# Performance work log

Hardware: AMD Instinct MI355X
Metric: run time of the kernel (lower is better)

The kernel has to match this reference:

```python
import jax, jax.numpy as jnp
import numpy as np

PH, PW = 7, 7      # pool_shape
SCALE = 1.0        # spatial_scale of PrRoIPool2D


def _tent_int(t):
    """Antiderivative of the bilinear tent kernel max(0, 1-|t|), clipped.
    Integral of tent from -inf to t."""
    t = jnp.clip(t, -1.0, 1.0)
    return jnp.where(t < 0.0, 0.5 * (t + 1.0) ** 2, 1.0 - 0.5 * (1.0 - t) ** 2)


def _axis_weights(lo, hi, n_bins, size):
    """Exact per-pixel integration weights along one axis.
    lo, hi: [R] roi edges. Returns (w [R, n_bins, size], bin_size [R]).
    w[r,k,i] = integral over bin k of tent(x - i) dx, so that
    sum_i F[i] * w[r,k,i] is the exact integral of the linearly
    interpolated signal F over bin k (Precise RoI Pooling)."""
    binsz = (hi - lo) / n_bins                       # [R]
    k = jnp.arange(n_bins, dtype=lo.dtype)
    a = lo[:, None] + k[None, :] * binsz[:, None]    # [R, n_bins] bin starts
    b = a + binsz[:, None]                           # bin ends
    i = jnp.arange(size, dtype=lo.dtype)             # pixel coordinates
    w = _tent_int(b[:, :, None] - i[None, None, :]) - _tent_int(a[:, :, None] - i[None, None, :])
    return w, binsz


def setup_inputs() -> dict:
    key = jax.random.key(0)
    k1, k2, k3, k4, k5 = jax.random.split(key, 5)
    B, C, H, W = 8, 64, 64, 64
    N = 512  # rois per leading dim; total R = N * B = 4096
    feature = jax.random.normal(k1, (B, C, H, W), dtype=jnp.float32)
    bidx = jax.random.randint(k2, (N, B, 1, 1), 0, B).astype(jnp.float32)
    x1 = jax.random.uniform(k3, (N, B, 1, 1), minval=0.0, maxval=W - 12.0)
    y1 = jax.random.uniform(k4, (N, B, 1, 1), minval=0.0, maxval=H - 12.0)
    wh = jax.random.uniform(k5, (N, B, 1, 1, 2), minval=4.0, maxval=12.0)
    x2 = x1 + wh[..., 0]
    y2 = y1 + wh[..., 1]
    rois = jnp.stack([bidx, x1, y1, x2, y2], axis=-1)  # [N, B, 1, 1, 5]
    return {"feature": feature, "rois": rois}


def reference(feature, rois):
    B, C, H, W = feature.shape
    # rois.permute([1,0,2,3,4]).reshape(-1, 5)
    r = jnp.transpose(rois, (1, 0, 2, 3, 4)).reshape(-1, 5)  # [R, 5]
    bidx = r[:, 0].astype(jnp.int32)
    x1 = r[:, 1] * SCALE
    y1 = r[:, 2] * SCALE
    x2 = r[:, 3] * SCALE
    y2 = r[:, 4] * SCALE

    wx, bw = _axis_weights(x1, x2, PW, W)  # [R, PW, W], [R]
    wy, bh = _axis_weights(y1, y2, PH, H)  # [R, PH, H], [R]

    # Route each ROI to its feature-batch entry without materializing
    # a [R, C, H, W] gather: fold the batch one-hot into the y-weights.
    onehot = (bidx[:, None] == jnp.arange(B)[None, :]).astype(feature.dtype)  # [R, B]
    wy_b = wy[:, :, None, :] * onehot[:, None, :, None]                      # [R, PH, B, H]

    tmp = jnp.einsum('rubi,bcij->rucj', wy_b, feature)  # [R, PH, C, W]
    integ = jnp.einsum('rucj,rvj->rcuv', tmp, wx)       # [R, C, PH, PW]

    area = jnp.maximum(bw * bh, 0.0)[:, None, None, None]
    bins = jnp.where(area > 0, integ / jnp.maximum(area, 1e-12), 0.0)

    # AvgPool2d(pool_shape) over the full (PH, PW) grid -> [R, C, 1, 1]
    out = jnp.mean(bins, axis=(2, 3), keepdims=True)
    return out
```

## Files before the change

kernel.cpp:

```cpp
#include <hip/hip_runtime.h>

constexpr int B = 8, C = 64, H = 64, W = 64;
constexpr int N = 512;
constexpr int R = N * B;
constexpr int HW = H * W;

__device__ __forceinline__ float tent_int(float t) {
    t = fminf(1.0f, fmaxf(-1.0f, t));
    float u = t + 1.0f;
    float v = 1.0f - t;
    return (t < 0.0f) ? 0.5f * u * u : 1.0f - 0.5f * v * v;
}

__global__ __launch_bounds__(256) void transpose_kernel(
    const float* __restrict__ in,
    float* __restrict__ out)
{
    __shared__ float tile[64][65];
    const int b  = blockIdx.x >> 6;
    const int tp = (blockIdx.x & 63) * 64;
    const int t  = threadIdx.x;
    const int tq = t >> 6;
    const int tl = t & 63;

    const float* src = in + (size_t)b * C * HW;
    #pragma unroll
    for (int s = 0; s < 16; ++s) {
        int c = s * 4 + tq;
        tile[c][tl] = src[(size_t)c * HW + tp + tl];
    }
    __syncthreads();
    float* dst = out + ((size_t)b * HW + tp) * C;
    #pragma unroll
    for (int s = 0; s < 16; ++s) {
        int p = s * 4 + tq;
        dst[(size_t)p * C + tl] = tile[tl][p];
    }
}

__global__ __launch_bounds__(256) void prroi_main(
    const float* __restrict__ ft,
    const float* __restrict__ rois,
    float* __restrict__ out)
{
    const int r    = blockIdx.x * 4 + (threadIdx.x >> 6);
    const int lane = threadIdx.x & 63;
    const int pg   = lane >> 4;
    const int cg   = lane & 15;

    const int bo = r >> 9;
    const int n  = r & 511;
    const float* rp = rois + ((size_t)n * B + bo) * 5;

    const int   b  = (int)rp[0];
    const float x1 = rp[1], y1 = rp[2], x2 = rp[3], y2 = rp[4];

    int i_lo = max(0, (int)ceilf(y1 - 1.0f));
    int i_hi = min(H - 1, (int)floorf(y2 + 1.0f));
    int j_lo = max(0, (int)ceilf(x1 - 1.0f));
    int j_hi = min(W - 1, (int)floorf(x2 + 1.0f));
    const int ny = i_hi - i_lo + 1;
    const int nx = j_hi - j_lo + 1;
    const int nk = (nx + 3) >> 2;

    float wx[4];
    int   coff[4];
    #pragma unroll
    for (int k = 0; k < 4; ++k) {
        int  jj    = k * 4 + pg;
        int  j     = j_lo + jj;
        bool valid = (jj < nx);
        float jf   = (float)j;
        wx[k]   = valid ? (tent_int(x2 - jf) - tent_int(x1 - jf)) : 0.0f;
        int jc  = min(j, W - 1);
        coff[k] = jc * C + cg * 4;
    }

    float4 acc = make_float4(0.0f, 0.0f, 0.0f, 0.0f);
    const float* fb = ft + (size_t)b * HW * C;
    for (int ii = 0; ii < ny; ++ii) {
        const int i  = i_lo + ii;
        const float fi = (float)i;
        const float wy = tent_int(y2 - fi) - tent_int(y1 - fi);
        const float* rowp = fb + (size_t)i * (W * C);
        #pragma unroll 4
        for (int k = 0; k < nk; ++k) {
            float4 v = *reinterpret_cast<const float4*>(rowp + coff[k]);
            float  w = wy * wx[k];
            acc.x = fmaf(w, v.x, acc.x);
            acc.y = fmaf(w, v.y, acc.y);
            acc.z = fmaf(w, v.z, acc.z);
            acc.w = fmaf(w, v.w, acc.w);
        }
    }

    acc.x += __shfl_xor(acc.x, 16); acc.y += __shfl_xor(acc.y, 16);
    acc.z += __shfl_xor(acc.z, 16); acc.w += __shfl_xor(acc.w, 16);
    acc.x += __shfl_xor(acc.x, 32); acc.y += __shfl_xor(acc.y, 32);
    acc.z += __shfl_xor(acc.z, 32); acc.w += __shfl_xor(acc.w, 32);

    const float prod  = (x2 - x1) * (y2 - y1);
    const float scale = (prod > 0.0f) ? (1.0f / fmaxf(prod, 49e-12f)) : 0.0f;

    if (pg == 0) {
        float4 res = make_float4(acc.x * scale, acc.y * scale,
                                 acc.z * scale, acc.w * scale);
        *reinterpret_cast<float4*>(out + (size_t)r * C + cg * 4) = res;
    }
}

__global__ __launch_bounds__(64) void prroi_fallback(
    const float* __restrict__ feature, const float* __restrict__ rois,
    float* __restrict__ out)
{
    const int r  = blockIdx.x;
    const int bo = r / N;
    const int n  = r - bo * N;
    const float* rp = rois + ((size_t)n * B + bo) * 5;
    const float x1 = rp[1], y1 = rp[2], x2 = rp[3], y2 = rp[4];
    const int b = (int)rp[0];
    int i_lo = max(0, (int)ceilf(y1 - 1.0f));
    int i_hi = min(H - 1, (int)floorf(y2 + 1.0f));
    int j_lo = max(0, (int)ceilf(x1 - 1.0f));
    int j_hi = min(W - 1, (int)floorf(x2 + 1.0f));
    const int ny = i_hi - i_lo + 1;
    const int nx = j_hi - j_lo + 1;
    __shared__ float sWy[16], sWx[16];
    const int t = threadIdx.x;
    if (t < 16) {
        int i = i_lo + t;
        sWy[t] = (t < ny) ? (tent_int(y2 - (float)i) - tent_int(y1 - (float)i)) : 0.0f;
    } else if (t < 32) {
        int tt = t - 16, j = j_lo + tt;
        sWx[tt] = (tt < nx) ? (tent_int(x2 - (float)j) - tent_int(x1 - (float)j)) : 0.0f;
    }
    __syncthreads();
    const float* fb = feature + ((size_t)b * C + t) * HW;
    float acc = 0.0f;
    for (int ii = 0; ii < ny; ++ii) {
        const float* row = fb + (size_t)(i_lo + ii) * W + j_lo;
        float rowsum = 0.0f;
        for (int jj = 0; jj < nx; ++jj) rowsum = fmaf(sWx[jj], row[jj], rowsum);
        acc = fmaf(sWy[ii], rowsum, acc);
    }
    const float bw = (x2 - x1) * (1.0f / 7.0f), bh = (y2 - y1) * (1.0f / 7.0f);
    const float area = fmaxf(bw * bh, 0.0f);
    out[(size_t)r * C + t] = (area > 0.0f) ? (acc / (49.0f * fmaxf(area, 1e-12f))) : 0.0f;
}

extern "C" void kernel_launch(void* const* d_in, const int* in_sizes, int n_in,
                              void* d_out, int out_size, void* d_ws, size_t ws_size,
                              hipStream_t stream) {
    const float* feature = (const float*)d_in[0];
    const float* rois    = (const float*)d_in[1];
    float* out           = (float*)d_out;

    const size_t need = (size_t)B * C * HW * sizeof(float);
    if (ws_size >= need) {
        float* ft = (float*)d_ws;
        transpose_kernel<<<B * (HW / 64), 256, 0, stream>>>(feature, ft);
        prroi_main<<<R / 4, 256, 0, stream>>>(ft, rois, out);
    } else {
        prroi_fallback<<<R, 64, 0, stream>>>(feature, rois, out);
    }
}
```

Measured before the change: 81.76 us.

## Bucket ROIs by batch index so each XCD reads one feature image

The prep kernel now also scans the ROIs and builds per-batch index lists with shared-memory atomics. The main kernel picks its bucket from blockIdx & 7, so each block processes only ROIs from one batch image. With round-robin block dispatch across XCDs, each XCD's L2 should then hold a single 1 MB feature slice instead of all eight. The cost is an extra serial ROI scan in eight of the prep blocks and many early-exit blocks in the main launch. Each bucket is silently capped at 768 ROIs, so skewed inputs would drop work.

```diff
diff --git a/kernel.cpp b/kernel.cpp
--- a/kernel.cpp
+++ b/kernel.cpp
@@ -4,6 +4,7 @@
 constexpr int N = 512;
 constexpr int R = N * B;
 constexpr int HW = H * W;
+constexpr int MAXB = 768;
 
 __device__ __forceinline__ float tent_int(float t) {
     t = fminf(1.0f, fmaxf(-1.0f, t));
@@ -12,11 +13,33 @@
     return (t < 0.0f) ? 0.5f * u * u : 1.0f - 0.5f * v * v;
 }
 
-__global__ __launch_bounds__(256) void transpose_kernel(
+__global__ __launch_bounds__(256) void prep_kernel(
     const float* __restrict__ in,
-    float* __restrict__ out)
+    const float* __restrict__ rois,
+    float* __restrict__ out,
+    int* __restrict__ counts,
+    int* __restrict__ idx)
 {
     __shared__ float tile[64][65];
+    __shared__ int cnt;
+
+    if (blockIdx.x < 8) {
+        if (threadIdx.x == 0) cnt = 0;
+        __syncthreads();
+        const int b = blockIdx.x;
+        for (int r = threadIdx.x; r < R; r += 256) {
+            const int bo = r >> 9, n = r & 511;
+            const int bi = (int)rois[((size_t)n * B + bo) * 5];
+            if (bi == b) {
+                int p = atomicAdd(&cnt, 1);
+                if (p < MAXB) idx[b * MAXB + p] = r;
+            }
+        }
+        __syncthreads();
+        if (threadIdx.x == 0) counts[b] = min(cnt, MAXB);
+        __syncthreads();
+    }
+
     const int b  = blockIdx.x >> 6;
     const int tp = (blockIdx.x & 63) * 64;
     const int t  = threadIdx.x;
@@ -41,9 +64,15 @@
 __global__ __launch_bounds__(256) void prroi_main(
     const float* __restrict__ ft,
     const float* __restrict__ rois,
+    const int* __restrict__ counts,
+    const int* __restrict__ idx,
     float* __restrict__ out)
 {
-    const int r    = blockIdx.x * 4 + (threadIdx.x >> 6);
+    const int bucket = blockIdx.x & 7;
+    const int slot   = (blockIdx.x >> 3) * 4 + (threadIdx.x >> 6);
+    if (slot >= counts[bucket]) return;
+    const int r = idx[bucket * MAXB + slot];
+
     const int lane = threadIdx.x & 63;
     const int pg   = lane >> 4;
     const int cg   = lane & 15;
@@ -51,9 +80,8 @@
     const int bo = r >> 9;
     const int n  = r & 511;
     const float* rp = rois + ((size_t)n * B + bo) * 5;
-
-    const int   b  = (int)rp[0];
     const float x1 = rp[1], y1 = rp[2], x2 = rp[3], y2 = rp[4];
+    const int b = bucket;
 
     int i_lo = max(0, (int)ceilf(y1 - 1.0f));
     int i_hi = min(H - 1, (int)floorf(y2 + 1.0f));
@@ -155,11 +183,14 @@
     const float* rois    = (const float*)d_in[1];
     float* out           = (float*)d_out;
 
-    const size_t need = (size_t)B * C * HW * sizeof(float);
+    const size_t ft_bytes  = (size_t)B * C * HW * sizeof(float);
+    const size_t need      = ft_bytes + 32 + (size_t)8 * MAXB * sizeof(int);
     if (ws_size >= need) {
-        float* ft = (float*)d_ws;
-        transpose_kernel<<<B * (HW / 64), 256, 0, stream>>>(feature, ft);
-        prroi_main<<<R / 4, 256, 0, stream>>>(ft, rois, out);
+        float* ft   = (float*)d_ws;
+        int* counts = (int*)((char*)d_ws + ft_bytes);
+        int* idx    = (int*)((char*)d_ws + ft_bytes + 32);
+        prep_kernel<<<B * (HW / 64), 256, 0, stream>>>(feature, rois, ft, counts, idx);
+        prroi_main<<<8 * (MAXB / 4), 256, 0, stream>>>(ft, rois, counts, idx, out);
     } else {
         prroi_fallback<<<R, 64, 0, stream>>>(feature, rois, out);
     }
```

Result: slower. 85.10 us (+4.1%).
